# Kernel optimization log

Hardware: AMD Instinct MI355X
Metric: run time of the kernel (lower is better)

## Reference

```python
import jax, jax.numpy as jnp
import numpy as np

EPS = 1e-5
N, K, CIN, COUT = 100000, 27, 64, 128


def sparse_conv(x, nbr, W):
    # x: [N, C]; nbr: [N, K] with sentinel index N meaning 'no neighbor'
    x_pad = jnp.concatenate([x, jnp.zeros((1, x.shape[1]), x.dtype)], axis=0)  # [N+1, C]
    g = x_pad[nbr]  # gather: [N, K, C]
    return jnp.einsum('nkc,kcd->nd', g, W)  # per-offset GEMM, scatter to output sites


def bn_relu(y, gamma, beta):
    # BatchNorm over active sites (training-mode batch statistics), then ReLU
    mu = y.mean(axis=0)
    var = y.var(axis=0)
    return jax.nn.relu((y - mu) * jax.lax.rsqrt(var + EPS) * gamma + beta)


def setup_inputs() -> dict:
    key = jax.random.key(0)
    ks = jax.random.split(key, 5)
    x = jax.random.normal(ks[0], (N, CIN), dtype=jnp.float32)
    # sentinel N indicates missing neighbor (maps to zero-padded row)
    nbr = jax.random.randint(ks[1], (N, K), 0, N + 1)
    W1 = jax.random.normal(ks[2], (K, CIN, COUT), dtype=jnp.float32) * (1.0 / np.sqrt(K * CIN))
    W2 = jax.random.normal(ks[3], (K, COUT, COUT), dtype=jnp.float32) * (1.0 / np.sqrt(K * COUT))
    W_skip = jax.random.normal(ks[4], (CIN, COUT), dtype=jnp.float32) * (1.0 / np.sqrt(CIN))
    return {
        'x': x, 'nbr': nbr,
        'W1': W1, 'gamma1': jnp.ones((COUT,), jnp.float32), 'beta1': jnp.zeros((COUT,), jnp.float32),
        'W2': W2, 'gamma2': jnp.ones((COUT,), jnp.float32), 'beta2': jnp.zeros((COUT,), jnp.float32),
        'W_skip': W_skip,
    }


def reference(x, nbr, W1, gamma1, beta1, W2, gamma2, beta2, W_skip):
    identity = x @ W_skip                      # 1x1 conv skip (same coords)
    h = bn_relu(sparse_conv(x, nbr, W1), gamma1, beta1)
    h = bn_relu(sparse_conv(h, nbr, W2), gamma2, beta2)
    return h + identity
```

## Files before the change

### kernel.cpp

```cpp
#include <hip/hip_runtime.h>
#include <hip/hip_bf16.h>

#define NSITES 100000
#define KOFFS 27
#define CIN 64
#define COUT 128

typedef unsigned short u16;
typedef __attribute__((ext_vector_type(8))) short s16x8;
typedef __attribute__((ext_vector_type(4))) float f32x4;

static __device__ __forceinline__ u16 f2bf(float f) {
    union { float f; unsigned u; } x; x.f = f;
    return (u16)((x.u + 0x7FFFu + ((x.u >> 16) & 1u)) >> 16);
}
static __device__ __forceinline__ float bf2f(u16 v) {
    union { unsigned u; float f; } x; x.u = ((unsigned)v) << 16;
    return x.f;
}

__global__ void prep_kernel(const float* __restrict__ W1, const float* __restrict__ W2,
                            const float* __restrict__ Wsk,
                            u16* __restrict__ W1t, u16* __restrict__ W2t,
                            u16* __restrict__ Wskt, float* __restrict__ zero_area) {
    int i = blockIdx.x * 256 + threadIdx.x;
    if (i < 27 * 64 * 128) {
        int k = i / 8192, r = i & 8191, d = r >> 6, c = r & 63;
        W1t[i] = f2bf(W1[k * 8192 + c * 128 + d]);
        return;
    }
    i -= 27 * 64 * 128;
    if (i < 27 * 128 * 128) {
        int k = i / 16384, r = i & 16383, d = r >> 7, c = r & 127;
        W2t[i] = f2bf(W2[k * 16384 + c * 128 + d]);
        return;
    }
    i -= 27 * 128 * 128;
    if (i < 8192) {
        int d = i >> 6, c = i & 63;
        Wskt[i] = f2bf(Wsk[c * 128 + d]);
        return;
    }
    i -= 8192;
    zero_area[i] = 0.0f;
}

__global__ void convert_x_kernel(const float* __restrict__ x, u16* __restrict__ xb) {
    long long e = ((long long)blockIdx.x * 256 + threadIdx.x) * 8;
    if (e >= (long long)(NSITES + 1) * CIN) return;
    s16x8 o;
    if (e < (long long)NSITES * CIN) {
        float4 v0 = *(const float4*)(x + e);
        float4 v1 = *(const float4*)(x + e + 4);
        o[0] = (short)f2bf(v0.x); o[1] = (short)f2bf(v0.y);
        o[2] = (short)f2bf(v0.z); o[3] = (short)f2bf(v0.w);
        o[4] = (short)f2bf(v1.x); o[5] = (short)f2bf(v1.y);
        o[6] = (short)f2bf(v1.z); o[7] = (short)f2bf(v1.w);
    } else {
#pragma unroll
        for (int j = 0; j < 8; ++j) o[j] = 0;
    }
    *(s16x8*)(xb + e) = o;
}

template <int CK, bool IDENT_FUSE, bool STATS>
__global__ __launch_bounds__(256, 3) void conv_kernel(
    const u16* __restrict__ xin, const int* __restrict__ nbr,
    const u16* __restrict__ Wt, u16* __restrict__ yout,
    float* __restrict__ psum, float* __restrict__ psq, int nk,
    const u16* __restrict__ Wskt, float* __restrict__ outid) {
    constexpr int STRIDE = CK + 8;
    constexpr int KSTEPS = CK / 32;
    constexpr int CPR = CK / 8;
    constexpr int RPP = 256 / CPR;
    constexpr int NPASS = 64 / RPP;
    __shared__ __align__(16) u16 a_tile[64 * STRIDE];
    __shared__ int nbr_tile[64 * KOFFS];

    const int tid = threadIdx.x;
    const int wave = tid >> 6;
    const int lane = tid & 63;
    const int m = lane & 15;
    const int q = lane >> 4;
    const int n0 = blockIdx.x * 64;
    const int wc = wave * 32;
    const int srow = tid / CPR;
    const int schunk = tid % CPR;

    for (int i = tid; i < 64 * KOFFS; i += 256) {
        int r = i / KOFFS;
        int kk = i - r * KOFFS;
        int row = n0 + r;
        nbr_tile[i] = (row < NSITES) ? nbr[row * KOFFS + kk] : NSITES;
    }
    __syncthreads();

    f32x4 acc[4][2];
#pragma unroll
    for (int rt = 0; rt < 4; ++rt)
#pragma unroll
        for (int ct = 0; ct < 2; ++ct)
#pragma unroll
            for (int r = 0; r < 4; ++r) acc[rt][ct][r] = 0.0f;

    s16x8 ag0[NPASS], ag1[NPASS];
#pragma unroll
    for (int p = 0; p < NPASS; ++p) {
        int r = p * RPP + srow;
        ag0[p] = *(const s16x8*)(xin + (long long)nbr_tile[r * KOFFS] * CK + schunk * 8);
    }
    if (nk > 1) {
#pragma unroll
        for (int p = 0; p < NPASS; ++p) {
            int r = p * RPP + srow;
            ag1[p] = *(const s16x8*)(xin + (long long)nbr_tile[r * KOFFS + 1] * CK + schunk * 8);
        }
    }

    auto conv_iter = [&](int k, s16x8 (&agc)[NPASS]) {
        s16x8 bf[2][KSTEPS];
        const u16* wb = Wt + (long long)k * (COUT * CK);
#pragma unroll
        for (int ct = 0; ct < 2; ++ct)
#pragma unroll
            for (int ks = 0; ks < KSTEPS; ++ks)
                bf[ct][ks] = *(const s16x8*)(wb + (wc + ct * 16 + m) * CK + ks * 32 + q * 8);

#pragma unroll
        for (int p = 0; p < NPASS; ++p)
            *(s16x8*)(a_tile + (p * RPP + srow) * STRIDE + schunk * 8) = agc[p];

        if (k + 2 < nk) {
#pragma unroll
            for (int p = 0; p < NPASS; ++p) {
                int r = p * RPP + srow;
                agc[p] = *(const s16x8*)(xin + (long long)nbr_tile[r * KOFFS + k + 2] * CK + schunk * 8);
            }
        }
        __syncthreads();

#pragma unroll
        for (int ks = 0; ks < KSTEPS; ++ks) {
            s16x8 af[4];
#pragma unroll
            for (int rt = 0; rt < 4; ++rt)
                af[rt] = *(const s16x8*)(a_tile + (rt * 16 + m) * STRIDE + ks * 32 + q * 8);
#pragma unroll
            for (int rt = 0; rt < 4; ++rt)
#pragma unroll
                for (int ct = 0; ct < 2; ++ct)
                    acc[rt][ct] = __builtin_amdgcn_mfma_f32_16x16x32_bf16(
                        af[rt], bf[ct][ks], acc[rt][ct], 0, 0, 0);
        }
        __syncthreads();
    };

    for (int k = 0; k < nk; k += 2) {
        conv_iter(k, ag0);
        if (k + 1 < nk) conv_iter(k + 1, ag1);
    }

#pragma unroll
    for (int rt = 0; rt < 4; ++rt) {
        int rowb = n0 + rt * 16 + q * 4;
#pragma unroll
        for (int ct = 0; ct < 2; ++ct) {
            int col = wc + ct * 16 + m;
#pragma unroll
            for (int r = 0; r < 4; ++r) {
                int row = rowb + r;
                if (row < NSITES) yout[(long long)row * COUT + col] = f2bf(acc[rt][ct][r]);
            }
        }
    }

    if (STATS) {
#pragma unroll
        for (int ct = 0; ct < 2; ++ct) {
            float s = 0.f, ss = 0.f;
#pragma unroll
            for (int rt = 0; rt < 4; ++rt)
#pragma unroll
                for (int r = 0; r < 4; ++r) {
                    float v = acc[rt][ct][r];
                    s += v; ss += v * v;
                }
            s += __shfl_xor(s, 16); ss += __shfl_xor(ss, 16);
            s += __shfl_xor(s, 32); ss += __shfl_xor(ss, 32);
            if (q == 0) {
                int col = wc + ct * 16 + m;
                int slot = blockIdx.x & 63;
                atomicAdd(psum + slot * COUT + col, s);
                atomicAdd(psq + slot * COUT + col, ss);
            }
        }
    }

    if (IDENT_FUSE) {
#pragma unroll
        for (int rt = 0; rt < 4; ++rt)
#pragma unroll
            for (int ct = 0; ct < 2; ++ct)
#pragma unroll
                for (int r = 0; r < 4; ++r) acc[rt][ct][r] = 0.0f;
        s16x8 aid[NPASS];
#pragma unroll
        for (int p = 0; p < NPASS; ++p) {
            int row = n0 + p * RPP + srow;
            long long idx = (row < NSITES) ? row : NSITES;
            aid[p] = *(const s16x8*)(xin + idx * CK + schunk * 8);
        }
        s16x8 bfi[2][KSTEPS];
#pragma unroll
        for (int ct = 0; ct < 2; ++ct)
#pragma unroll
            for (int ks = 0; ks < KSTEPS; ++ks)
                bfi[ct][ks] = *(const s16x8*)(Wskt + (wc + ct * 16 + m) * CK + ks * 32 + q * 8);
#pragma unroll
        for (int p = 0; p < NPASS; ++p)
            *(s16x8*)(a_tile + (p * RPP + srow) * STRIDE + schunk * 8) = aid[p];
        __syncthreads();
#pragma unroll
        for (int ks = 0; ks < KSTEPS; ++ks) {
            s16x8 af[4];
#pragma unroll
            for (int rt = 0; rt < 4; ++rt)
                af[rt] = *(const s16x8*)(a_tile + (rt * 16 + m) * STRIDE + ks * 32 + q * 8);
#pragma unroll
            for (int rt = 0; rt < 4; ++rt)
#pragma unroll
                for (int ct = 0; ct < 2; ++ct)
                    acc[rt][ct] = __builtin_amdgcn_mfma_f32_16x16x32_bf16(
                        af[rt], bfi[ct][ks], acc[rt][ct], 0, 0, 0);
        }
#pragma unroll
        for (int rt = 0; rt < 4; ++rt) {
            int rowb = n0 + rt * 16 + q * 4;
#pragma unroll
            for (int ct = 0; ct < 2; ++ct) {
                int col = wc + ct * 16 + m;
#pragma unroll
                for (int r = 0; r < 4; ++r) {
                    int row = rowb + r;
                    if (row < NSITES) outid[(long long)row * COUT + col] = acc[rt][ct][r];
                }
            }
        }
    }
}

__global__ void bn_stats_kernel(const float* __restrict__ psum, const float* __restrict__ psq,
                                const float* __restrict__ gamma, const float* __restrict__ beta,
                                float* __restrict__ ab) {
    int col = threadIdx.x;
    float s = 0.f, ss = 0.f;
    for (int i = 0; i < 64; ++i) { s += psum[i * COUT + col]; ss += psq[i * COUT + col]; }
    const float inv_n = 1.0f / (float)NSITES;
    float mu = s * inv_n;
    float var = ss * inv_n - mu * mu;
    float rs = rsqrtf(var + 1e-5f);
    float a = gamma[col] * rs;
    ab[col] = a;
    ab[COUT + col] = beta[col] - mu * a;
}

__global__ void bn_apply_kernel(const u16* __restrict__ y, const float* __restrict__ ab,
                                u16* __restrict__ h) {
    long long e = ((long long)blockIdx.x * 256 + threadIdx.x) * 8;
    if (e >= (long long)(NSITES + 1) * COUT) return;
    s16x8 o;
    if (e < (long long)NSITES * COUT) {
        int cb = (int)(e & (COUT - 1));
        s16x8 v = *(const s16x8*)(y + e);
#pragma unroll
        for (int j = 0; j < 8; ++j) {
            float r = bf2f((u16)v[j]) * ab[cb + j] + ab[COUT + cb + j];
            o[j] = (short)f2bf(fmaxf(r, 0.f));
        }
    } else {
#pragma unroll
        for (int j = 0; j < 8; ++j) o[j] = 0;
    }
    *(s16x8*)(h + e) = o;
}

__global__ void final_kernel(const u16* __restrict__ y, const float* __restrict__ ab,
                             float* __restrict__ out) {
    long long e = ((long long)blockIdx.x * 256 + threadIdx.x) * 8;
    if (e >= (long long)NSITES * COUT) return;
    int cb = (int)(e & (COUT - 1));
    s16x8 v = *(const s16x8*)(y + e);
    float4 i0 = *(const float4*)(out + e);
    float4 i1 = *(const float4*)(out + e + 4);
    float is[8] = {i0.x, i0.y, i0.z, i0.w, i1.x, i1.y, i1.z, i1.w};
    float os[8];
#pragma unroll
    for (int j = 0; j < 8; ++j) {
        float r = bf2f((u16)v[j]) * ab[cb + j] + ab[COUT + cb + j];
        os[j] = fmaxf(r, 0.f) + is[j];
    }
    *(float4*)(out + e) = make_float4(os[0], os[1], os[2], os[3]);
    *(float4*)(out + e + 4) = make_float4(os[4], os[5], os[6], os[7]);
}

extern "C" void kernel_launch(void* const* d_in, const int* in_sizes, int n_in,
                              void* d_out, int out_size, void* d_ws, size_t ws_size,
                              hipStream_t stream) {
    const float* x   = (const float*)d_in[0];
    const int*   nbr = (const int*)d_in[1];
    const float* W1  = (const float*)d_in[2];
    const float* g1  = (const float*)d_in[3];
    const float* b1  = (const float*)d_in[4];
    const float* W2  = (const float*)d_in[5];
    const float* g2  = (const float*)d_in[6];
    const float* b2  = (const float*)d_in[7];
    const float* Wsk = (const float*)d_in[8];
    float* out = (float*)d_out;

    char* ws = (char*)d_ws;
    u16*   xb   = (u16*)(ws);
    u16*   W1t  = (u16*)(ws + 12800128);
    u16*   W2t  = (u16*)(ws + 13242496);
    u16*   Wskt = (u16*)(ws + 14127232);
    u16*   y    = (u16*)(ws + 14143616);
    u16*   h1   = (u16*)(ws + 39743616);
    float* ps1  = (float*)(ws + 65343872);
    float* pq1  = ps1 + 8192;
    float* ps2  = pq1 + 8192;
    float* pq2  = ps2 + 8192;
    float* ab1  = pq2 + 8192;
    float* ab2  = ab1 + 256;

    const int NBLK = (NSITES + 63) / 64;

    prep_kernel<<<2752, 256, 0, stream>>>(W1, W2, Wsk, W1t, W2t, Wskt, ps1);
    convert_x_kernel<<<3126, 256, 0, stream>>>(x, xb);
    conv_kernel<64, true, true><<<NBLK, 256, 0, stream>>>(xb, nbr, W1t, y, ps1, pq1, KOFFS, Wskt, out);
    bn_stats_kernel<<<1, 128, 0, stream>>>(ps1, pq1, g1, b1, ab1);
    bn_apply_kernel<<<6251, 256, 0, stream>>>(y, ab1, h1);
    conv_kernel<128, false, true><<<NBLK, 256, 0, stream>>>(h1, nbr, W2t, y, ps2, pq2, KOFFS, nullptr, nullptr);
    bn_stats_kernel<<<1, 128, 0, stream>>>(ps2, pq2, g2, b2, ab2);
    final_kernel<<<6250, 256, 0, stream>>>(y, ab2, out);
}
```

Baseline: 456.1 us.

## Double-buffer gathered A tile in LDS with one barrier per offset

Replaces the two-register-set prefetch scheme (two gathers in flight, two barriers per offset) with a double-buffered LDS A tile. Each offset's gather is issued before the MFMA work on the current buffer and written to the other buffer afterward, so only one barrier per offset is needed. Launch bounds are raised to 4 blocks per SM for the CIN=64 instantiation to improve occupancy. The trade-off is less prefetch depth (one gather in flight instead of two), more LDS per block, and tighter register limits.

```diff
diff --git a/kernel.cpp b/kernel.cpp
--- a/kernel.cpp
+++ b/kernel.cpp
@@ -64,7 +64,7 @@
 }
 
 template <int CK, bool IDENT_FUSE, bool STATS>
-__global__ __launch_bounds__(256, 3) void conv_kernel(
+__global__ __launch_bounds__(256, (CK == 64 ? 4 : 3)) void conv_kernel(
     const u16* __restrict__ xin, const int* __restrict__ nbr,
     const u16* __restrict__ Wt, u16* __restrict__ yout,
     float* __restrict__ psum, float* __restrict__ psq, int nk,
@@ -74,7 +74,7 @@
     constexpr int CPR = CK / 8;
     constexpr int RPP = 256 / CPR;
     constexpr int NPASS = 64 / RPP;
-    __shared__ __align__(16) u16 a_tile[64 * STRIDE];
+    __shared__ __align__(16) u16 a_tile[2][64 * STRIDE];
     __shared__ int nbr_tile[64 * KOFFS];
 
     const int tid = threadIdx.x;
@@ -103,21 +103,30 @@
 #pragma unroll
             for (int r = 0; r < 4; ++r) acc[rt][ct][r] = 0.0f;
 
-    s16x8 ag0[NPASS], ag1[NPASS];
+    s16x8 ag[NPASS];
 #pragma unroll
     for (int p = 0; p < NPASS; ++p) {
         int r = p * RPP + srow;
-        ag0[p] = *(const s16x8*)(xin + (long long)nbr_tile[r * KOFFS] * CK + schunk * 8);
-    }
-    if (nk > 1) {
-#pragma unroll
-        for (int p = 0; p < NPASS; ++p) {
-            int r = p * RPP + srow;
-            ag1[p] = *(const s16x8*)(xin + (long long)nbr_tile[r * KOFFS + 1] * CK + schunk * 8);
-        }
-    }
-
-    auto conv_iter = [&](int k, s16x8 (&agc)[NPASS]) {
+        ag[p] = *(const s16x8*)(xin + (long long)nbr_tile[r * KOFFS] * CK + schunk * 8);
+    }
+#pragma unroll
+    for (int p = 0; p < NPASS; ++p)
+        *(s16x8*)(a_tile[0] + (p * RPP + srow) * STRIDE + schunk * 8) = ag[p];
+    __syncthreads();
+
+    for (int k = 0; k < nk; ++k) {
+        const u16* abuf = a_tile[k & 1];
+        u16* wbuf = a_tile[(k + 1) & 1];
+        const bool more = (k + 1 < nk);
+
+        if (more) {
+#pragma unroll
+            for (int p = 0; p < NPASS; ++p) {
+                int r = p * RPP + srow;
+                ag[p] = *(const s16x8*)(xin + (long long)nbr_tile[r * KOFFS + k + 1] * CK + schunk * 8);
+            }
+        }
+
         s16x8 bf[2][KSTEPS];
         const u16* wb = Wt + (long long)k * (COUT * CK);
 #pragma unroll
@@ -127,24 +136,11 @@
                 bf[ct][ks] = *(const s16x8*)(wb + (wc + ct * 16 + m) * CK + ks * 32 + q * 8);
 
 #pragma unroll
-        for (int p = 0; p < NPASS; ++p)
-            *(s16x8*)(a_tile + (p * RPP + srow) * STRIDE + schunk * 8) = agc[p];
-
-        if (k + 2 < nk) {
-#pragma unroll
-            for (int p = 0; p < NPASS; ++p) {
-                int r = p * RPP + srow;
-                agc[p] = *(const s16x8*)(xin + (long long)nbr_tile[r * KOFFS + k + 2] * CK + schunk * 8);
-            }
-        }
-        __syncthreads();
-
-#pragma unroll
         for (int ks = 0; ks < KSTEPS; ++ks) {
             s16x8 af[4];
 #pragma unroll
             for (int rt = 0; rt < 4; ++rt)
-                af[rt] = *(const s16x8*)(a_tile + (rt * 16 + m) * STRIDE + ks * 32 + q * 8);
+                af[rt] = *(const s16x8*)(abuf + (rt * 16 + m) * STRIDE + ks * 32 + q * 8);
 #pragma unroll
             for (int rt = 0; rt < 4; ++rt)
 #pragma unroll
@@ -152,12 +148,13 @@
                     acc[rt][ct] = __builtin_amdgcn_mfma_f32_16x16x32_bf16(
                         af[rt], bf[ct][ks], acc[rt][ct], 0, 0, 0);
         }
+
+        if (more) {
+#pragma unroll
+            for (int p = 0; p < NPASS; ++p)
+                *(s16x8*)(wbuf + (p * RPP + srow) * STRIDE + schunk * 8) = ag[p];
+        }
         __syncthreads();
-    };
-
-    for (int k = 0; k < nk; k += 2) {
-        conv_iter(k, ag0);
-        if (k + 1 < nk) conv_iter(k + 1, ag1);
     }
 
 #pragma unroll
@@ -218,14 +215,14 @@
                 bfi[ct][ks] = *(const s16x8*)(Wskt + (wc + ct * 16 + m) * CK + ks * 32 + q * 8);
 #pragma unroll
         for (int p = 0; p < NPASS; ++p)
-            *(s16x8*)(a_tile + (p * RPP + srow) * STRIDE + schunk * 8) = aid[p];
+            *(s16x8*)(a_tile[0] + (p * RPP + srow) * STRIDE + schunk * 8) = aid[p];
         __syncthreads();
 #pragma unroll
         for (int ks = 0; ks < KSTEPS; ++ks) {
             s16x8 af[4];
 #pragma unroll
             for (int rt = 0; rt < 4; ++rt)
-                af[rt] = *(const s16x8*)(a_tile + (rt * 16 + m) * STRIDE + ks * 32 + q * 8);
+                af[rt] = *(const s16x8*)(a_tile[0] + (rt * 16 + m) * STRIDE + ks * 32 + q * 8);
 #pragma unroll
             for (int rt = 0; rt < 4; ++rt)
 #pragma unroll
```

Result: slower. 467.9 us (+2.6%).
